# Kernel optimization log

Measured on AMD Instinct MI355X. Metric: run time of the kernel, lower is better.

## Reference

```python
import jax, jax.numpy as jnp
import numpy as np
import math

B, S = 2, 2048
DIM_MODEL = 2048
NUM_Q_HEADS = 16
GROUP_SIZE = 4
NUM_KV_HEADS = NUM_Q_HEADS // GROUP_SIZE
DIM_K = 128
RMS_EPS = 1e-6
ROPE_BASE = 10000.0


def setup_inputs() -> dict:
    key = jax.random.key(0)
    ks = jax.random.split(key, 8)
    x = jax.random.normal(ks[0], (B, S, DIM_MODEL), dtype=jnp.float32)
    mask = jnp.tril(jnp.ones((S, S), dtype=bool))  # causal
    # Linear weights stored as [in, out] so y = x @ W (bias=False everywhere)
    sd = 1.0 / math.sqrt(DIM_MODEL)
    Wq = jax.random.uniform(ks[1], (DIM_MODEL, DIM_K * NUM_Q_HEADS), jnp.float32, -sd, sd)
    Wk = jax.random.uniform(ks[2], (DIM_MODEL, DIM_K * NUM_KV_HEADS), jnp.float32, -sd, sd)
    Wv = jax.random.uniform(ks[3], (DIM_MODEL, DIM_K * NUM_KV_HEADS), jnp.float32, -sd, sd)
    sf = 1.0 / math.sqrt(DIM_K * NUM_Q_HEADS)
    Wfc = jax.random.uniform(ks[4], (DIM_K * NUM_Q_HEADS, DIM_MODEL), jnp.float32, -sf, sf)
    q_gamma = jnp.ones((DIM_K,), dtype=jnp.float32)
    k_gamma = jnp.ones((DIM_K,), dtype=jnp.float32)
    return {"x": x, "mask": mask, "Wq": Wq, "Wk": Wk, "Wv": Wv,
            "Wfc": Wfc, "q_gamma": q_gamma, "k_gamma": k_gamma}


def _rope(t):
    # t: [B, H, S, D], rotate-half RoPE
    d = t.shape[-1]
    half = d // 2
    inv_freq = 1.0 / (ROPE_BASE ** (jnp.arange(half, dtype=jnp.float32) / half))
    pos = jnp.arange(t.shape[2], dtype=jnp.float32)
    ang = pos[:, None] * inv_freq[None, :]            # [S, half]
    cos, sin = jnp.cos(ang), jnp.sin(ang)              # [S, half]
    t1, t2 = t[..., :half], t[..., half:]
    return jnp.concatenate([t1 * cos - t2 * sin, t2 * cos + t1 * sin], axis=-1)


def _rmsnorm(t, gamma):
    ms = jnp.mean(t * t, axis=-1, keepdims=True)
    return t * jax.lax.rsqrt(ms + RMS_EPS) * gamma


def reference(x, mask, Wq, Wk, Wv, Wfc, q_gamma, k_gamma):
    b, s, _ = x.shape
    q = (x @ Wq).reshape(b, s, NUM_Q_HEADS, DIM_K).transpose(0, 2, 1, 3)   # [B,Hq,S,D]
    k = (x @ Wk).reshape(b, s, NUM_KV_HEADS, DIM_K).transpose(0, 2, 1, 3)  # [B,Hkv,S,D]
    v = (x @ Wv).reshape(b, s, NUM_KV_HEADS, DIM_K).transpose(0, 2, 1, 3)
    q = _rmsnorm(_rope(q), q_gamma)
    k = _rmsnorm(_rope(k), k_gamma)
    q = q.reshape(b, NUM_KV_HEADS, GROUP_SIZE, s, DIM_K)                    # [B,Hkv,G,S,D]
    scores = jnp.einsum('bhgqd,bhkd->bhgqk', q, k) / math.sqrt(DIM_K)      # [B,Hkv,G,S,S]
    scores = jnp.where(mask, scores, -jnp.inf)
    attn = jax.nn.softmax(scores, axis=-1)  # dropout is identity in eval
    out = jnp.einsum('bhgqk,bhkd->bhgqd', attn, v)                          # [B,Hkv,G,S,D]
    out = out.reshape(b, NUM_Q_HEADS, s, DIM_K).transpose(0, 2, 1, 3)
    out = out.reshape(b, s, NUM_Q_HEADS * DIM_K) @ Wfc                      # [B,S,DM]
    return out
```

## Files before the change

### kernel.cpp

```cpp
#include <hip/hip_runtime.h>
#include <hip/hip_bf16.h>

typedef __attribute__((ext_vector_type(8))) short bf16x8;
typedef __attribute__((ext_vector_type(4))) short bf16x4;
typedef __attribute__((ext_vector_type(4))) float f32x4;

#define S_LEN 2048
#define DMODEL 2048
#define NQH 16
#define NKVH 4
#define DK 128

__device__ __forceinline__ float b2f(short u) {
  union { unsigned int i; float f; } x;
  x.i = ((unsigned int)(unsigned short)u) << 16;
  return x.f;
}
__device__ __forceinline__ short f2b(float f) {
  union { float f; unsigned int i; } x; x.f = f;
  unsigned int r = (x.i + 0x7fffu + ((x.i >> 16) & 1u)) >> 16;
  return (short)r;
}
__device__ __forceinline__ unsigned int cvtpk(float a, float b) {
  unsigned int r;
  asm("v_cvt_pk_bf16_f32 %0, %1, %2" : "=v"(r) : "v"(a), "v"(b));
  return r;
}
__device__ __forceinline__ f32x4 mfma16(bf16x8 a, bf16x8 b, f32x4 c) {
  return __builtin_amdgcn_mfma_f32_16x16x32_bf16(a, b, c, 0, 0, 0);
}
__device__ __forceinline__ void async16(short* lds, const short* g) {
  __builtin_amdgcn_global_load_lds(
      (const __attribute__((address_space(1))) unsigned int*)(const void*)g,
      (__attribute__((address_space(3))) unsigned int*)(void*)lds, 16, 0, 0);
}

__device__ __forceinline__ void transpose_tile(const float* __restrict__ in,
                                               short* __restrict__ out, int R, int C,
                                               int bx, int by, int tid, short (*t)[33]) {
  const int c0 = bx * 32, r0 = by * 32;
  const int tx = tid & 31, ty = tid >> 5;
#pragma unroll
  for (int i = 0; i < 32; i += 8)
    t[ty + i][tx] = f2b(in[(size_t)(r0 + ty + i) * C + c0 + tx]);
  __syncthreads();
#pragma unroll
  for (int i = 0; i < 32; i += 8)
    out[(size_t)(c0 + ty + i) * R + r0 + tx] = t[tx][ty + i];
}

__global__ __launch_bounds__(256) void prep_kernel(const float* __restrict__ x,
                                                   const float* __restrict__ Wq,
                                                   const float* __restrict__ Wk,
                                                   const float* __restrict__ Wv,
                                                   const float* __restrict__ Wfc,
                                                   short* __restrict__ xb,
                                                   short* __restrict__ WqT,
                                                   short* __restrict__ WkT,
                                                   short* __restrict__ WvT,
                                                   short* __restrict__ WfcT,
                                                   float* __restrict__ rt) {
  __shared__ short t[32][33];
  const int id = blockIdx.x;
  const int tid = threadIdx.x;
  if (id < 8192) {
    const int i = id * 256 + tid;
    float4 v = ((const float4*)x)[i];
    bf16x4 o;
    o[0] = f2b(v.x); o[1] = f2b(v.y); o[2] = f2b(v.z); o[3] = f2b(v.w);
    ((bf16x4*)xb)[i] = o;
  } else if (id < 12288) {
    const int r = id - 8192;
    transpose_tile(Wq, WqT, 2048, 2048, r & 63, r >> 6, tid, t);
  } else if (id < 13312) {
    const int r = id - 12288;
    transpose_tile(Wk, WkT, 2048, 512, r & 15, r >> 4, tid, t);
  } else if (id < 14336) {
    const int r = id - 13312;
    transpose_tile(Wv, WvT, 2048, 512, r & 15, r >> 4, tid, t);
  } else if (id < 18432) {
    const int r = id - 14336;
    transpose_tile(Wfc, WfcT, 2048, 2048, r & 63, r >> 6, tid, t);
  } else {
    const int i = (id - 18432) * 256 + tid;
    const int s = i >> 6, d = i & 63;
    float ang = (float)s * __expf((float)d * -0.14391157f);
    float c, sn;
    __sincosf(ang, &sn, &c);
    rt[s * 128 + d] = c;
    rt[s * 128 + 64 + d] = sn;
  }
}

__device__ __forceinline__ void stage_tile64(short* Ls, const short* Gb, int ldg,
                                             int w, int lane) {
#pragma unroll
  for (int i = 0; i < 4; ++i) {
    const int r0 = w * 32 + i * 8;
    const int row = r0 + (lane >> 3);
    const int colb = ((lane & 7) * 8) ^ ((row & 7) << 3);
    async16(Ls + r0 * 64, Gb + (size_t)row * ldg + colb);
  }
}

__global__ __launch_bounds__(256) void gemm_qkv(const short* __restrict__ A,
                                                const short* __restrict__ WT,
                                                short* __restrict__ Qr,
                                                short* __restrict__ Kr,
                                                short* __restrict__ Vtr,
                                                const float* __restrict__ qg,
                                                const float* __restrict__ kg,
                                                const float* __restrict__ ropeT) {
  constexpr int CS_LD = 136;
  __shared__ __align__(16) short smem[4 * 128 * 64];

  const int flat = blockIdx.x;
  const int xcd = flat & 7, idx = flat >> 3;
  const int mb = (xcd >> 1) * 8 + (idx & 7);
  const int nb = (xcd & 1) * 12 + (idx >> 3);

  const int tid = threadIdx.x;
  const int lane = tid & 63;
  const int w = tid >> 6;
  const int wm = w >> 1, wn = w & 1;
  const int l15 = lane & 15, lg = lane >> 4;
  const int K = DMODEL;
  constexpr int NSTEP = DMODEL / 64;

  f32x4 acc[4][4] = {};
  const short* Ab = A + (size_t)mb * 128 * K;
  const short* Bb = WT + (size_t)nb * 128 * K;

  stage_tile64(smem, Ab, K, w, lane);
  stage_tile64(smem + 8192, Bb, K, w, lane);
  asm volatile("s_waitcnt vmcnt(0)" ::: "memory");
  __syncthreads();

  for (int t = 0; t < NSTEP; ++t) {
    const int cur = t & 1;
    short* Ac = smem + cur * 16384;
    short* Bc = Ac + 8192;
    if (t + 1 < NSTEP) {
      short* An = smem + (cur ^ 1) * 16384;
      stage_tile64(An, Ab + (t + 1) * 64, K, w, lane);
      stage_tile64(An + 8192, Bb + (t + 1) * 64, K, w, lane);
    }
#pragma unroll
    for (int kk = 0; kk < 2; ++kk) {
      bf16x8 af[4], bfr[4];
#pragma unroll
      for (int mt = 0; mt < 4; ++mt)
        af[mt] = *(const bf16x8*)(Ac + (wm * 64 + mt * 16 + l15) * 64 +
                                  ((kk * 32 + lg * 8) ^ ((l15 & 7) << 3)));
#pragma unroll
      for (int nt = 0; nt < 4; ++nt)
        bfr[nt] = *(const bf16x8*)(Bc + (wn * 64 + nt * 16 + l15) * 64 +
                                   ((kk * 32 + lg * 8) ^ ((l15 & 7) << 3)));
#pragma unroll
      for (int mt = 0; mt < 4; ++mt)
#pragma unroll
        for (int nt = 0; nt < 4; ++nt)
          acc[mt][nt] = mfma16(af[mt], bfr[nt], acc[mt][nt]);
    }
    asm volatile("s_waitcnt vmcnt(0)" ::: "memory");
    __syncthreads();
  }

  short* Cs = smem;
#pragma unroll
  for (int mt = 0; mt < 4; ++mt)
#pragma unroll
    for (int nt = 0; nt < 4; ++nt)
#pragma unroll
      for (int r = 0; r < 4; ++r)
        Cs[(wm * 64 + mt * 16 + lg * 4 + r) * CS_LD + wn * 64 + nt * 16 + l15] =
            f2b(acc[mt][nt][r]);
  __syncthreads();

  const int srow0 = mb * 128;
  const int b = srow0 >> 11;

  if (nb < 20) {
    const bool isQ = nb < 16;
    const int h = isQ ? nb : nb - 16;
    const float* gamma = isQ ? qg : kg;
    const int r = tid >> 1, half = tid & 1;
    const int s = (srow0 + r) & 2047;
    const float* rt = ropeT + (size_t)s * 128;
    float ss = 0.f;
    bf16x8 ov[8];
#pragma unroll
    for (int j = 0; j < 8; ++j) {
      bf16x8 t1v = *(const bf16x8*)(Cs + r * CS_LD + j * 8);
      bf16x8 t2v = *(const bf16x8*)(Cs + r * CS_LD + 64 + j * 8);
      float4 c0 = *(const float4*)(rt + j * 8);
      float4 c1 = *(const float4*)(rt + j * 8 + 4);
      float4 s0 = *(const float4*)(rt + 64 + j * 8);
      float4 s1 = *(const float4*)(rt + 64 + j * 8 + 4);
      float cc[8] = {c0.x, c0.y, c0.z, c0.w, c1.x, c1.y, c1.z, c1.w};
      float sn[8] = {s0.x, s0.y, s0.z, s0.w, s1.x, s1.y, s1.z, s1.w};
#pragma unroll
      for (int i = 0; i < 8; ++i) {
        float t1 = b2f(t1v[i]), t2 = b2f(t2v[i]);
        float o = half ? (t2 * cc[i] + t1 * sn[i]) : (t1 * cc[i] - t2 * sn[i]);
        ss += o * o;
        ov[j][i] = f2b(o);
      }
    }
    ss += __shfl_xor(ss, 1);
    float inv = rsqrtf(ss * (1.0f / 128.0f) + 1e-6f);
    if (isQ) inv *= (0.08838834764831845f * 1.4426950408889634f);
    const int NH = isQ ? NQH : NKVH;
    short* outp = isQ ? Qr : Kr;
    short* ob = outp + ((size_t)(b * NH + h) * S_LEN + s) * DK + half * 64;
#pragma unroll
    for (int j = 0; j < 8; ++j) {
      float4 g0 = *(const float4*)(gamma + half * 64 + j * 8);
      float4 g1 = *(const float4*)(gamma + half * 64 + j * 8 + 4);
      float gg[8] = {g0.x, g0.y, g0.z, g0.w, g1.x, g1.y, g1.z, g1.w};
      bf16x8 vv;
#pragma unroll
      for (int i = 0; i < 8; ++i) vv[i] = f2b(b2f(ov[j][i]) * inv * gg[i]);
      *(bf16x8*)(ob + j * 8) = vv;
    }
  } else {
    const int h = nb - 20;
    const int d = tid & 127;
    const int sh = tid >> 7;
    const int sbase = (srow0 & 2047) + sh * 64;
    short* ob = Vtr + ((size_t)(b * NKVH + h) * DK + d) * S_LEN + sbase;
    for (int i0 = 0; i0 < 64; i0 += 8) {
      bf16x8 v;
#pragma unroll
      for (int j = 0; j < 8; ++j) {
        const int p = i0 + j;
        const int sl = sh * 64 + 16 * (p & 3) + (p >> 2);
        v[j] = Cs[sl * CS_LD + d];
      }
      *(bf16x8*)(ob + i0) = v;
    }
  }
}

__global__ __launch_bounds__(256) void gemm_out(const short* __restrict__ A,
                                                const short* __restrict__ BT,
                                                float* __restrict__ outf) {
  __shared__ __align__(16) short smem[4 * 128 * 64];

  const int flat = blockIdx.x;
  const int xcd = flat & 7, idx = flat >> 3;
  const int mb = (xcd >> 1) * 8 + (idx & 7);
  const int nb = (xcd & 1) * 8 + (idx >> 3);

  const int tid = threadIdx.x;
  const int lane = tid & 63;
  const int w = tid >> 6;
  const int wm = w >> 1, wn = w & 1;
  const int l15 = lane & 15, lg = lane >> 4;
  const int K = NQH * DK, N = DMODEL;
  constexpr int NSTEP = (NQH * DK) / 64;

  f32x4 acc[4][4] = {};
  const short* Ab = A + (size_t)mb * 128 * K;
  const short* Bb = BT + (size_t)nb * 128 * K;

  stage_tile64(smem, Ab, K, w, lane);
  stage_tile64(smem + 8192, Bb, K, w, lane);
  asm volatile("s_waitcnt vmcnt(0)" ::: "memory");
  __syncthreads();

  for (int t = 0; t < NSTEP; ++t) {
    const int cur = t & 1;
    short* Ac = smem + cur * 16384;
    short* Bc = Ac + 8192;
    if (t + 1 < NSTEP) {
      short* An = smem + (cur ^ 1) * 16384;
      stage_tile64(An, Ab + (t + 1) * 64, K, w, lane);
      stage_tile64(An + 8192, Bb + (t + 1) * 64, K, w, lane);
    }
#pragma unroll
    for (int kk = 0; kk < 2; ++kk) {
      bf16x8 af[4], bfr[4];
#pragma unroll
      for (int mt = 0; mt < 4; ++mt)
        af[mt] = *(const bf16x8*)(Ac + (wm * 64 + mt * 16 + l15) * 64 +
                                  ((kk * 32 + lg * 8) ^ ((l15 & 7) << 3)));
#pragma unroll
      for (int nt = 0; nt < 4; ++nt)
        bfr[nt] = *(const bf16x8*)(Bc + (wn * 64 + nt * 16 + l15) * 64 +
                                   ((kk * 32 + lg * 8) ^ ((l15 & 7) << 3)));
#pragma unroll
      for (int mt = 0; mt < 4; ++mt)
#pragma unroll
        for (int nt = 0; nt < 4; ++nt)
          acc[mt][nt] = mfma16(af[mt], bfr[nt], acc[mt][nt]);
    }
    asm volatile("s_waitcnt vmcnt(0)" ::: "memory");
    __syncthreads();
  }

#pragma unroll
  for (int mt = 0; mt < 4; ++mt) {
    const int row = mb * 128 + wm * 64 + mt * 16 + lg * 4;
#pragma unroll
    for (int nt = 0; nt < 4; ++nt) {
      const int col = nb * 128 + wn * 64 + nt * 16 + l15;
#pragma unroll
      for (int r = 0; r < 4; ++r)
        outf[(size_t)(row + r) * N + col] = acc[mt][nt][r];
    }
  }
}

__device__ __forceinline__ void stage_kv(const short* __restrict__ Kb,
                                         const short* __restrict__ Vb, int kb,
                                         short* Ks, short* Vs, int w, int lane) {
#pragma unroll
  for (int i = 0; i < 4; ++i) {
    const int c = 4 * w + i;
    const int krow = c * 4 + (lane >> 4);
    const int kcol = (((lane & 15) * 16) ^ ((krow & 7) << 4)) >> 1;
    async16(Ks + c * 512, Kb + (size_t)(kb + krow) * DK + kcol);
    const int vrow = c * 8 + (lane >> 3);
    const int vcol = (((lane & 7) * 16) ^ ((vrow & 7) << 4)) >> 1;
    async16(Vs + c * 512, Vb + (size_t)vrow * S_LEN + kb + vcol);
  }
}

__device__ __forceinline__ void sm_pv(f32x4* sc, float* lsum, f32x4* acco,
                                      const short* Vc, short* Pw, int q0, bool diag,
                                      int kb, int l15, int lg) {
  if (diag) {
#pragma unroll
    for (int nt = 0; nt < 4; ++nt) {
      const int k = kb + nt * 16 + l15;
#pragma unroll
      for (int r = 0; r < 4; ++r)
        if (k > q0 + lg * 4 + r) sc[nt][r] = -1e30f;
    }
  }
#pragma unroll
  for (int r = 0; r < 4; ++r) {
    const float p0 = exp2f(sc[0][r]);
    const float p1 = exp2f(sc[1][r]);
    const float p2 = exp2f(sc[2][r]);
    const float p3 = exp2f(sc[3][r]);
    lsum[r] += (p0 + p1) + (p2 + p3);
    uint2 dv;
    dv.x = cvtpk(p0, p1);
    dv.y = cvtpk(p2, p3);
    *(uint2*)(Pw + (lg * 4 + r) * 72 + l15 * 4) = dv;
  }
#pragma unroll
  for (int kk = 0; kk < 2; ++kk) {
    bf16x8 ap = *(const bf16x8*)(Pw + l15 * 72 + kk * 32 + lg * 8);
#pragma unroll
    for (int dt = 0; dt < 8; ++dt) {
      const int vrow = dt * 16 + l15;
      bf16x8 bv = *(const bf16x8*)(Vc + vrow * 64 +
                                   (((kk * 64 + lg * 16) ^ ((vrow & 7) << 4)) >> 1));
      acco[dt] = mfma16(ap, bv, acco[dt]);
    }
  }
}

__device__ __forceinline__ void attn_writeout(f32x4* acco, float* lsum,
                                              short* __restrict__ AO, int b, int qh,
                                              int q0, int l15, int lg) {
  float ls[4];
#pragma unroll
  for (int r = 0; r < 4; ++r) {
    float t = lsum[r];
    t += __shfl_xor(t, 1);
    t += __shfl_xor(t, 2);
    t += __shfl_xor(t, 4);
    t += __shfl_xor(t, 8);
    ls[r] = 1.0f / t;
  }
  short* ob = AO + (size_t)(b * S_LEN + q0) * (NQH * DK) + qh * DK;
#pragma unroll
  for (int dt = 0; dt < 8; ++dt)
#pragma unroll
    for (int r = 0; r < 4; ++r)
      ob[(size_t)(lg * 4 + r) * (NQH * DK) + dt * 16 + l15] = f2b(acco[dt][r] * ls[r]);
}

__global__ __launch_bounds__(256, 2) void attn_kernel(const short* __restrict__ Qr,
                                                      const short* __restrict__ Kr,
                                                      const short* __restrict__ Vt,
                                                      short* __restrict__ AO) {
  const int flat = blockIdx.x;
  const int nw = (flat & 7) * 64 + (flat >> 3);
  const int qtA = nw & 15;
  const int bh = nw >> 4;
  const int qtB = 31 - qtA;
  const int b = bh >> 4, qh = bh & 15;
  const int kvh = qh >> 2;
  const short* Qb = Qr + (size_t)bh * S_LEN * DK;
  const short* Kb = Kr + (size_t)(b * NKVH + kvh) * S_LEN * DK;
  const short* Vb = Vt + (size_t)(b * NKVH + kvh) * DK * S_LEN;
  const int tid = threadIdx.x, lane = tid & 63, w = tid >> 6;
  const int l15 = lane & 15, lg = lane >> 4;

  __shared__ __align__(16) short KV[4][64 * 128];
  __shared__ __align__(16) short P[4][16][72];
  short* Pw = &P[w][0][0];

  const int q0A = qtA * 64 + w * 16, q0B = qtB * 64 + w * 16;
  bf16x8 aqA[4], aqB[4];
#pragma unroll
  for (int kk = 0; kk < 4; ++kk) {
    aqA[kk] = *(const bf16x8*)(Qb + (size_t)(q0A + l15) * DK + kk * 32 + lg * 8);
    aqB[kk] = *(const bf16x8*)(Qb + (size_t)(q0B + l15) * DK + kk * 32 + lg * 8);
  }

  f32x4 accoA[8] = {}, accoB[8] = {};
  float lsA[4] = {0.f, 0.f, 0.f, 0.f}, lsB[4] = {0.f, 0.f, 0.f, 0.f};

  short* Kcur = KV[0]; short* Vcur = KV[1];
  short* Knxt = KV[2]; short* Vnxt = KV[3];

  stage_kv(Kb, Vb, 0, Kcur, Vcur, w, lane);
  asm volatile("s_waitcnt vmcnt(0)" ::: "memory");
  __syncthreads();

  for (int kt = 0; kt <= qtB; ++kt) {
    const int kb = kt * 64;
    if (kt < qtB) stage_kv(Kb, Vb, kb + 64, Knxt, Vnxt, w, lane);

    if (kt <= qtA) {
      f32x4 scB[4] = {}, scA[4] = {};
#pragma unroll
      for (int kk = 0; kk < 4; ++kk)
#pragma unroll
        for (int nt = 0; nt < 4; ++nt) {
          const int krow = nt * 16 + l15;
          bf16x8 bk = *(const bf16x8*)(Kcur + krow * 128 +
                                       (((kk * 64 + lg * 16) ^ ((krow & 7) << 4)) >> 1));
          scB[nt] = mfma16(aqB[kk], bk, scB[nt]);
          scA[nt] = mfma16(aqA[kk], bk, scA[nt]);
        }
      sm_pv(scB, lsB, accoB, Vcur, Pw, q0B, false, kb, l15, lg);
      sm_pv(scA, lsA, accoA, Vcur, Pw, q0A, kt == qtA, kb, l15, lg);
    } else {
      f32x4 scB[4] = {};
#pragma unroll
      for (int kk = 0; kk < 4; ++kk)
#pragma unroll
        for (int nt = 0; nt < 4; ++nt) {
          const int krow = nt * 16 + l15;
          bf16x8 bk = *(const bf16x8*)(Kcur + krow * 128 +
                                       (((kk * 64 + lg * 16) ^ ((krow & 7) << 4)) >> 1));
          scB[nt] = mfma16(aqB[kk], bk, scB[nt]);
        }
      sm_pv(scB, lsB, accoB, Vcur, Pw, q0B, kt == qtB, kb, l15, lg);
    }

    asm volatile("s_waitcnt vmcnt(0)" ::: "memory");
    __syncthreads();
    short* t;
    t = Kcur; Kcur = Knxt; Knxt = t;
    t = Vcur; Vcur = Vnxt; Vnxt = t;
  }

  attn_writeout(accoB, lsB, AO, b, qh, q0B, l15, lg);
  attn_writeout(accoA, lsA, AO, b, qh, q0A, l15, lg);
}

extern "C" void kernel_launch(void* const* d_in, const int* in_sizes, int n_in,
                              void* d_out, int out_size, void* d_ws, size_t ws_size,
                              hipStream_t stream) {
  const float* x = (const float*)d_in[0];
  const float* Wq = (const float*)d_in[2];
  const float* Wk = (const float*)d_in[3];
  const float* Wv = (const float*)d_in[4];
  const float* Wfc = (const float*)d_in[5];
  const float* qg = (const float*)d_in[6];
  const float* kg = (const float*)d_in[7];

  short* ws = (short*)d_ws;
  short* xb = ws;
  short* WqkvT = xb + (size_t)4096 * 2048;
  short* WqT = WqkvT;
  short* WkT = WqT + (size_t)2048 * 2048;
  short* WvT = WkT + (size_t)512 * 2048;
  short* WfcT = WvT + (size_t)512 * 2048;
  short* Qr = WfcT + (size_t)2048 * 2048;
  short* Kr = Qr + (size_t)32 * 2048 * 128;
  short* Vt = Kr + (size_t)8 * 2048 * 128;
  float* ropeT = (float*)(Vt + (size_t)8 * 128 * 2048);
  short* AO = xb;

  prep_kernel<<<18944, 256, 0, stream>>>(x, Wq, Wk, Wv, Wfc, xb, WqT, WkT, WvT,
                                         WfcT, ropeT);

  gemm_qkv<<<768, 256, 0, stream>>>(xb, WqkvT, Qr, Kr, Vt, qg, kg, ropeT);

  attn_kernel<<<512, 256, 0, stream>>>(Qr, Kr, Vt, AO);

  gemm_out<<<512, 256, 0, stream>>>(AO, WfcT, (float*)d_out);
}
```

Measured before the change: 189.3 us.

## Split QKV GEMM K-tiles into half-steps with finer-grained async pipelining

```diff
diff --git a/kernel.cpp b/kernel.cpp
--- a/kernel.cpp
+++ b/kernel.cpp
@@ -103,6 +103,91 @@
   }
 }
 
+__device__ __forceinline__ void kcore128(const short* __restrict__ Ab,
+                                         const short* __restrict__ Bb,
+                                         short* sm, f32x4 (&acc)[4][4],
+                                         int w, int lane, int wm, int wn,
+                                         int l15, int lg) {
+  const int K = 2048;
+  const int srow = 32 * w + (lane >> 2);
+  const int colp = (((lane & 3) ^ ((srow >> 1) & 3)) * 8);
+  const short* pA0 = Ab + (size_t)srow * K + colp;
+  const short* pA1 = pA0 + (size_t)16 * K;
+  const short* pB0 = Bb + (size_t)srow * K + colp;
+  const short* pB1 = pB0 + (size_t)16 * K;
+  const int sdst = w * 1024;
+  const int perm = (l15 >> 1) & 3;
+  const int aoff = (wm * 64 + l15) * 32 + ((lg ^ perm) * 8);
+  const int boff = 8192 + (wn * 64 + l15) * 32 + ((lg ^ perm) * 8);
+
+  auto stage = [&](int bufn, int tn, int h) {
+    short* d = sm + bufn * 16384 + h * 4096 + sdst;
+    const int off = tn * 64 + h * 32;
+    async16(d, pA0 + off);
+    async16(d + 512, pA1 + off);
+    async16(d + 8192, pB0 + off);
+    async16(d + 8192 + 512, pB1 + off);
+  };
+  auto half = [&](int bc, int h) {
+    const short* base = sm + bc * 16384 + h * 4096;
+    bf16x8 af[4], bfr[4];
+#pragma unroll
+    for (int mt = 0; mt < 4; ++mt) af[mt] = *(const bf16x8*)(base + aoff + mt * 512);
+#pragma unroll
+    for (int nt = 0; nt < 4; ++nt) bfr[nt] = *(const bf16x8*)(base + boff + nt * 512);
+#pragma unroll
+    for (int mt = 0; mt < 4; ++mt)
+#pragma unroll
+      for (int nt = 0; nt < 4; ++nt)
+        acc[mt][nt] = mfma16(af[mt], bfr[nt], acc[mt][nt]);
+  };
+
+  stage(0, 0, 0);
+  stage(0, 0, 1);
+
+#pragma unroll 1
+  for (int tt = 0; tt < 30; tt += 2) {
+    asm volatile("s_waitcnt vmcnt(4)" ::: "memory");
+    __builtin_amdgcn_s_barrier();
+    asm volatile("" ::: "memory");
+    stage(1, tt + 1, 0);
+    half(0, 0);
+    asm volatile("s_waitcnt vmcnt(4)" ::: "memory");
+    __builtin_amdgcn_s_barrier();
+    asm volatile("" ::: "memory");
+    stage(1, tt + 1, 1);
+    half(0, 1);
+    asm volatile("s_waitcnt vmcnt(4)" ::: "memory");
+    __builtin_amdgcn_s_barrier();
+    asm volatile("" ::: "memory");
+    stage(0, tt + 2, 0);
+    half(1, 0);
+    asm volatile("s_waitcnt vmcnt(4)" ::: "memory");
+    __builtin_amdgcn_s_barrier();
+    asm volatile("" ::: "memory");
+    stage(0, tt + 2, 1);
+    half(1, 1);
+  }
+  asm volatile("s_waitcnt vmcnt(4)" ::: "memory");
+  __builtin_amdgcn_s_barrier();
+  asm volatile("" ::: "memory");
+  stage(1, 31, 0);
+  half(0, 0);
+  asm volatile("s_waitcnt vmcnt(4)" ::: "memory");
+  __builtin_amdgcn_s_barrier();
+  asm volatile("" ::: "memory");
+  stage(1, 31, 1);
+  half(0, 1);
+  asm volatile("s_waitcnt vmcnt(4)" ::: "memory");
+  __builtin_amdgcn_s_barrier();
+  asm volatile("" ::: "memory");
+  half(1, 0);
+  asm volatile("s_waitcnt vmcnt(0)" ::: "memory");
+  __builtin_amdgcn_s_barrier();
+  asm volatile("" ::: "memory");
+  half(1, 1);
+}
+
 __global__ __launch_bounds__(256) void gemm_qkv(const short* __restrict__ A,
                                                 const short* __restrict__ WT,
                                                 short* __restrict__ Qr,
@@ -112,7 +197,7 @@
                                                 const float* __restrict__ kg,
                                                 const float* __restrict__ ropeT) {
   constexpr int CS_LD = 136;
-  __shared__ __align__(16) short smem[4 * 128 * 64];
+  __shared__ __align__(16) short smem[32768];
 
   const int flat = blockIdx.x;
   const int xcd = flat & 7, idx = flat >> 3;
@@ -125,47 +210,12 @@
   const int wm = w >> 1, wn = w & 1;
   const int l15 = lane & 15, lg = lane >> 4;
   const int K = DMODEL;
-  constexpr int NSTEP = DMODEL / 64;
 
   f32x4 acc[4][4] = {};
-  const short* Ab = A + (size_t)mb * 128 * K;
-  const short* Bb = WT + (size_t)nb * 128 * K;
-
-  stage_tile64(smem, Ab, K, w, lane);
-  stage_tile64(smem + 8192, Bb, K, w, lane);
-  asm volatile("s_waitcnt vmcnt(0)" ::: "memory");
+  kcore128(A + (size_t)mb * 128 * K, WT + (size_t)nb * 128 * K, smem, acc,
+           w, lane, wm, wn, l15, lg);
+
   __syncthreads();
-
-  for (int t = 0; t < NSTEP; ++t) {
-    const int cur = t & 1;
-    short* Ac = smem + cur * 16384;
-    short* Bc = Ac + 8192;
-    if (t + 1 < NSTEP) {
-      short* An = smem + (cur ^ 1) * 16384;
-      stage_tile64(An, Ab + (t + 1) * 64, K, w, lane);
-      stage_tile64(An + 8192, Bb + (t + 1) * 64, K, w, lane);
-    }
-#pragma unroll
-    for (int kk = 0; kk < 2; ++kk) {
-      bf16x8 af[4], bfr[4];
-#pragma unroll
-      for (int mt = 0; mt < 4; ++mt)
-        af[mt] = *(const bf16x8*)(Ac + (wm * 64 + mt * 16 + l15) * 64 +
-                                  ((kk * 32 + lg * 8) ^ ((l15 & 7) << 3)));
-#pragma unroll
-      for (int nt = 0; nt < 4; ++nt)
-        bfr[nt] = *(const bf16x8*)(Bc + (wn * 64 + nt * 16 + l15) * 64 +
-                                   ((kk * 32 + lg * 8) ^ ((l15 & 7) << 3)));
-#pragma unroll
-      for (int mt = 0; mt < 4; ++mt)
-#pragma unroll
-        for (int nt = 0; nt < 4; ++nt)
-          acc[mt][nt] = mfma16(af[mt], bfr[nt], acc[mt][nt]);
-    }
-    asm volatile("s_waitcnt vmcnt(0)" ::: "memory");
-    __syncthreads();
-  }
-
   short* Cs = smem;
 #pragma unroll
   for (int mt = 0; mt < 4; ++mt)
```

Result: no change. 189.3 us (+0.0%).
